# Performance work log

Measured on AMD Instinct MI355X. Metric: run time of the kernel, lower is better.

The kernel has to match this reference:

```python
import jax, jax.numpy as jnp
import numpy as np

PI = float(np.pi)
EPS = 1e-7


def conv2d(x, w, b, pad=0):
    y = jax.lax.conv_general_dilated(x, w, (1, 1), [(pad, pad), (pad, pad)],
                                     dimension_numbers=('NCHW', 'OIHW', 'NCHW'))
    return y + b[None, :, None, None]


def nearest_resize(x, oh, ow):
    # PyTorch F.interpolate(mode='nearest'): src_idx = floor(dst_idx * in/out)
    ih, iw = x.shape[-2], x.shape[-1]
    ri = (jnp.arange(oh) * ih) // oh
    ci = (jnp.arange(ow) * iw) // ow
    return x[:, :, ri, :][:, :, :, ci]


def maxpool_to(x, oh, ow):
    # adaptive_max_pool2d with divisible sizes == strided max pool
    b, c, h, w = x.shape
    return x.reshape(b, c, oh, h // oh, ow, w // ow).max(axis=(3, 5))


def minmax(t):
    # per-sample min-max normalization over (channel,h,w)
    mn = t.min(axis=(1, 2, 3), keepdims=True)
    mx = t.max(axis=(1, 2, 3), keepdims=True)
    return (t - mn) / (mx - mn + EPS)


def nonlocal2d(x, g_w, g_b, th_w, th_b, ph_w, ph_b, out_w, out_b):
    # embedded-Gaussian NonLocal2D, reduction=1, use_scale=False
    b, c, h, w = x.shape
    g_x = conv2d(x, g_w, g_b).reshape(b, c, h * w).transpose(0, 2, 1)    # (b, hw, c)
    th = conv2d(x, th_w, th_b).reshape(b, c, h * w).transpose(0, 2, 1)   # (b, hw, c)
    ph = conv2d(x, ph_w, ph_b).reshape(b, c, h * w)                      # (b, c, hw)
    pw = jax.nn.softmax(jnp.einsum('bic,bcj->bij', th, ph), axis=-1)     # (b, hw, hw)
    y = jnp.einsum('bij,bjc->bic', pw, g_x).transpose(0, 2, 1).reshape(b, c, h, w)
    return x + conv2d(y, out_w, out_b)


def reference(x0, x1, x2, x3, x4, rc_w, rc_b,
              nl_g_w, nl_g_b, nl_theta_w, nl_theta_b,
              nl_phi_w, nl_phi_b, nl_out_w, nl_out_b):
    inputs = [x0, x1, x2, x3, x4]
    refine_level = 2
    gh, gw = inputs[refine_level].shape[2:]
    feats = []
    for i, x in enumerate(inputs):
        if i < refine_level:
            feats.append(maxpool_to(x, gh, gw))
        else:
            feats.append(nearest_resize(x, gh, gw))
    ori_fe = sum(feats) / len(feats)
    bsf = nonlocal2d(ori_fe, nl_g_w, nl_g_b, nl_theta_w, nl_theta_b,
                     nl_phi_w, nl_phi_b, nl_out_w, nl_out_b)

    outs = []
    for i, x in enumerate(inputs):
        b, c, h, w = x.shape
        # ConvModule(C->1, 3x3, relu) then extra F.relu (idempotent)
        basic_map = jax.nn.relu(conv2d(x, rc_w[i], rc_b[i], pad=1))      # (b,1,h,w)
        row = x.mean(axis=3)[:, 0, :]                                     # (b,h)
        col = x.mean(axis=2)[:, 0, :]                                     # (b,w)
        avg_map = minmax((row[:, :, None] * col[:, None, :])[:, None])    # (b,1,h,w)
        basic_reg = minmax(basic_map)
        distance_map = jnp.cos((avg_map - basic_reg) * (PI / 2))
        attention = jax.nn.relu(nearest_resize(bsf, h, w) * distance_map)
        outs.append(x + attention)
    return tuple(outs)


def setup_inputs() -> dict:
    key = jax.random.key(0)
    ks = jax.random.split(key, 16)
    C = 256
    sizes = [200, 100, 50, 25, 13]
    inp = {}
    for i, s in enumerate(sizes):
        inp[f'x{i}'] = jax.random.normal(ks[i], (4, C, s, s), dtype=jnp.float32)
    inp['rc_w'] = jax.random.normal(ks[5], (5, 1, C, 3, 3), dtype=jnp.float32) * 0.02
    inp['rc_b'] = jnp.zeros((5, 1), dtype=jnp.float32)
    inp['nl_g_w'] = jax.random.normal(ks[6], (C, C, 1, 1), dtype=jnp.float32) * 0.02
    inp['nl_g_b'] = jnp.zeros((C,), dtype=jnp.float32)
    inp['nl_theta_w'] = jax.random.normal(ks[7], (C, C, 1, 1), dtype=jnp.float32) * 0.02
    inp['nl_theta_b'] = jnp.zeros((C,), dtype=jnp.float32)
    inp['nl_phi_w'] = jax.random.normal(ks[8], (C, C, 1, 1), dtype=jnp.float32) * 0.02
    inp['nl_phi_b'] = jnp.zeros((C,), dtype=jnp.float32)
    inp['nl_out_w'] = jax.random.normal(ks[9], (C, C, 1, 1), dtype=jnp.float32) * 0.02
    inp['nl_out_b'] = jnp.zeros((C,), dtype=jnp.float32)
    return inp
```

## Files before the change

kernel.cpp:

```cpp
#include <hip/hip_runtime.h>
#include <math.h>

typedef __attribute__((ext_vector_type(8))) short short8;
typedef __attribute__((ext_vector_type(4))) float f32x4;
typedef __attribute__((ext_vector_type(2))) float f32x2;
typedef __attribute__((ext_vector_type(4))) unsigned short u16x4;

#define EPSV 1e-7f
#define PI_2 1.57079632679489662f
#define NEG_BIG (-3.4e38f)

constexpr int B = 4, C = 256;
constexpr int GW = 50;
constexpr int PR = 2500, PP = 2560;
constexpr int CPP = C * PP;
constexpr long long SPB = (long long)PP * PP;
constexpr int PS = PP * C;
constexpr int ZT = 213176;

constexpr size_t OFF_ORI   = 0;
constexpr size_t OFF_BSF   = OFF_ORI + (size_t)B * CPP;
constexpr size_t OFF_Z     = OFF_BSF + (size_t)B * CPP;
constexpr size_t OFF_BASIC = OFF_Z + (size_t)9 * ZT;
constexpr size_t OFF_ROW   = OFF_BASIC + 213184;
constexpr size_t OFF_COL   = OFF_ROW + 1600;
constexpr size_t OFF_STATS = OFF_COL + 1600;
constexpr size_t OFF_RSUM  = OFF_STATS + 128;
constexpr size_t OFF_U16   = OFF_RSUM + 10240;
constexpr size_t U_ORIT = 0;
constexpr size_t U_THT  = U_ORIT + (size_t)B * CPP;
constexpr size_t U_PHT  = U_THT  + (size_t)B * CPP;
constexpr size_t U_G    = U_PHT  + (size_t)B * CPP;
constexpr size_t U_YTT  = U_G    + (size_t)B * CPP;
constexpr size_t U_WB   = U_YTT  + (size_t)B * CPP;

__device__ __forceinline__ unsigned short f2b(float x) {
    union { float f; unsigned u; } q{x};
    unsigned r = q.u + 0x7FFFu + ((q.u >> 16) & 1u);
    return (unsigned short)(r >> 16);
}
__device__ __forceinline__ float b2f(unsigned short u) {
    union { unsigned u; float f; } q{(unsigned)u << 16};
    return q.f;
}

__device__ __forceinline__ float orife_val(
    int idx, const float* __restrict__ x0, const float* __restrict__ x1,
    const float* __restrict__ x2, const float* __restrict__ x3,
    const float* __restrict__ x4)
{
    int p = idx % PP; int bc = idx / PP;
    if (p >= PR) return 0.0f;
    int y = p / GW, x = p % GW;
    const float* p0 = x0 + (size_t)bc * 40000;
    float m0 = NEG_BIG;
    #pragma unroll
    for (int dy = 0; dy < 4; dy++) {
        f32x4 r = *(const f32x4*)(p0 + (y * 4 + dy) * 200 + x * 4);
        m0 = fmaxf(m0, fmaxf(fmaxf(r[0], r[1]), fmaxf(r[2], r[3])));
    }
    const float* p1 = x1 + (size_t)bc * 10000;
    float m1 = fmaxf(fmaxf(p1[(y*2)*100 + x*2],   p1[(y*2)*100 + x*2+1]),
                     fmaxf(p1[(y*2+1)*100 + x*2], p1[(y*2+1)*100 + x*2+1]));
    float v2 = x2[(size_t)bc * 2500 + p];
    float v3 = x3[(size_t)bc * 625 + (y/2)*25 + (x/2)];
    int ry = (y * 13) / 50, rx = (x * 13) / 50;
    float v4 = x4[(size_t)bc * 169 + ry * 13 + rx];
    return (m0 + m1 + v2 + v3 + v4) * 0.2f;
}

constexpr int ORIFE_T = 2560 * 256;

__global__ __launch_bounds__(256) void k_pre(
    const float* __restrict__ x0, const float* __restrict__ x1,
    const float* __restrict__ x2, const float* __restrict__ x3,
    const float* __restrict__ x4, const float* __restrict__ rc_w,
    const float* __restrict__ wth, const float* __restrict__ wph,
    const float* __restrict__ wg,  const float* __restrict__ wout,
    unsigned short* __restrict__ wb, float* __restrict__ ori,
    float* __restrict__ z, float* __restrict__ row, float* __restrict__ col,
    float* __restrict__ rowsum)
{
    __shared__ float wsm[C * 12];
    const int bx = blockIdx.x;
    const int tid = threadIdx.x;

    if (bx < 388) {
        int rid = bx * 4 + (tid >> 6);
        int lane = tid & 63;
        int base, H; const float* x;
        if      (rid < 800)  { base = 0;    H = 200; x = x0; }
        else if (rid < 1200) { base = 800;  H = 100; x = x1; }
        else if (rid < 1400) { base = 1200; H = 50;  x = x2; }
        else if (rid < 1500) { base = 1400; H = 25;  x = x3; }
        else                 { base = 1500; H = 13;  x = x4; }
        int r = rid - base; int b = r / H, h = r - (r / H) * H;
        const float* xr = x + (size_t)b * C * H * H + (size_t)h * H;
        float s = 0.0f;
        for (int w = lane; w < H; w += 64) s += xr[w];
        #pragma unroll
        for (int off = 32; off > 0; off >>= 1) s += __shfl_down(s, off);
        if (lane == 0) row[rid] = s / (float)H;
    } else if (bx < 395) {
        int idx = (bx - 388) * 256 + tid;
        if (idx >= 1552) return;
        int base, H; const float* x;
        if      (idx < 800)  { base = 0;    H = 200; x = x0; }
        else if (idx < 1200) { base = 800;  H = 100; x = x1; }
        else if (idx < 1400) { base = 1200; H = 50;  x = x2; }
        else if (idx < 1500) { base = 1400; H = 25;  x = x3; }
        else                 { base = 1500; H = 13;  x = x4; }
        int r = idx - base; int b = r / H, w = r - (r / H) * H;
        const float* xc = x + (size_t)b * C * H * H + w;
        float s = 0.0f;
        int h = 0;
        for (; h + 3 < H; h += 4) {
            float a0 = xc[(size_t)h * H];
            float a1 = xc[(size_t)(h + 1) * H];
            float a2 = xc[(size_t)(h + 2) * H];
            float a3 = xc[(size_t)(h + 3) * H];
            s += (a0 + a1) + (a2 + a3);
        }
        for (; h < H; h++) s += xc[(size_t)h * H];
        col[idx] = s / (float)H;
    } else if (bx < 1419) {
        int idx = (bx - 395) * 256 + tid;
        int seg = idx >> 16, off = idx & 65535;
        const float* s = (seg == 0) ? wth : (seg == 1) ? wph : (seg == 2) ? wg : wout;
        wb[idx] = f2b(s[off]);
    } else if (bx < 1838) {
        int bxx = bx - 1419;
        int lvl, base, HW, PH, zb; const float* x;
        if      (bxx < 313) { lvl = 0; base = 0;   HW = 40000; PH = 20000; zb = 0;      x = x0; }
        else if (bxx < 392) { lvl = 1; base = 313; HW = 10000; PH = 5000;  zb = 160000; x = x1; }
        else if (bxx < 412) { lvl = 2; base = 392; HW = 2500;  PH = 1250;  zb = 200000; x = x2; }
        else if (bxx < 417) { lvl = 3; base = 412; HW = 625;   PH = 313;   zb = 210000; x = x3; }
        else                { lvl = 4; base = 417; HW = 169;   PH = 85;    zb = 212500; x = x4; }
        const bool alig = (HW & 1) == 0;

        const float* w9 = rc_w + (size_t)lvl * C * 9;
        for (int i = tid; i < C * 9; i += 256) wsm[(i / 9) * 12 + (i % 9)] = w9[i];
        __syncthreads();

        int idx = (bxx - base) * 256 + tid;
        if (idx >= B * PH) return;
        int b = idx / PH, pp = (idx - b * PH) * 2;
        bool has2 = (pp + 1 < HW);

        float acc0[9] = {}, acc1[9] = {};
        const float* xp = x + (size_t)b * C * HW + pp;
        for (int c0 = 0; c0 < C; c0 += 8) {
            float v0[8], v1[8];
            #pragma unroll
            for (int k = 0; k < 8; k++) {
                const float* a = xp + (size_t)(c0 + k) * HW;
                if (alig && has2) { f32x2 t = *(const f32x2*)a; v0[k] = t[0]; v1[k] = t[1]; }
                else { v0[k] = a[0]; v1[k] = has2 ? a[1] : 0.0f; }
            }
            #pragma unroll
            for (int k = 0; k < 8; k++) {
                const float* wc = &wsm[(c0 + k) * 12];
                f32x4 w0 = *(const f32x4*)wc;
                f32x4 w1 = *(const f32x4*)(wc + 4);
                float w8 = wc[8];
                acc0[0] += v0[k] * w0[0]; acc1[0] += v1[k] * w0[0];
                acc0[1] += v0[k] * w0[1]; acc1[1] += v1[k] * w0[1];
                acc0[2] += v0[k] * w0[2]; acc1[2] += v1[k] * w0[2];
                acc0[3] += v0[k] * w0[3]; acc1[3] += v1[k] * w0[3];
                acc0[4] += v0[k] * w1[0]; acc1[4] += v1[k] * w1[0];
                acc0[5] += v0[k] * w1[1]; acc1[5] += v1[k] * w1[1];
                acc0[6] += v0[k] * w1[2]; acc1[6] += v1[k] * w1[2];
                acc0[7] += v0[k] * w1[3]; acc1[7] += v1[k] * w1[3];
                acc0[8] += v0[k] * w8;    acc1[8] += v1[k] * w8;
            }
        }
        #pragma unroll
        for (int t = 0; t < 9; t++) {
            size_t o = (size_t)t * ZT + zb + (size_t)b * HW + pp;
            if (alig && has2) { f32x2 wv = {acc0[t], acc1[t]}; *(f32x2*)&z[o] = wv; }
            else { z[o] = acc0[t]; if (has2) z[o + 1] = acc1[t]; }
        }
    } else if (bx < 4398) {
        int t0 = (bx - 1838) * 256 + tid;
        #pragma unroll
        for (int k = 0; k < 4; k++) {
            int idx = t0 + k * ORIFE_T;
            ori[idx] = orife_val(idx, x0, x1, x2, x3, x4);
        }
    } else {
        int idx = (bx - 4398) * 1024 + tid * 4;
        f32x4 zv = {0.0f, 0.0f, 0.0f, 0.0f};
        *(f32x4*)(rowsum + idx) = zv;
    }
}

__global__ __launch_bounds__(256) void k_tcvt(const float* __restrict__ ori,
                                              unsigned short* __restrict__ ot)
{
    __shared__ unsigned short t[64][66];
    int p0 = blockIdx.x * 64, c0 = blockIdx.y * 64, b = blockIdx.z;
    int pp = threadIdx.x & 63, cb = threadIdx.x >> 6;
    #pragma unroll
    for (int i = 0; i < 16; i++) {
        int cc = cb * 16 + i;
        t[cc][pp] = f2b(ori[((size_t)b * C + c0 + cc) * PP + p0 + pp]);
    }
    __syncthreads();
    int cc2 = threadIdx.x & 63, pb = threadIdx.x >> 6;
    #pragma unroll
    for (int i = 0; i < 16; i++) {
        int pp2 = pb * 16 + i;
        ot[((size_t)b * PP + p0 + pp2) * C + c0 + cc2] = t[cc2][pp2];
    }
}

constexpr int LDT = 40;

__global__ __launch_bounds__(256) void k_proj(
    const unsigned short* __restrict__ wb, const unsigned short* __restrict__ orit,
    const float* __restrict__ th_b, const float* __restrict__ ph_b,
    const float* __restrict__ g_b,
    unsigned short* __restrict__ tht, unsigned short* __restrict__ pht,
    unsigned short* __restrict__ gb)
{
    __shared__ __align__(16) unsigned short As[128 * LDT];
    __shared__ __align__(16) unsigned short Bs[128 * LDT];

    const int z = blockIdx.z;
    const int b = z / 3, wsel = z - b * 3;
    const bool tp = (wsel < 2);
    const unsigned short* A = tp ? (orit + (size_t)b * CPP) : (wb + 131072);
    const unsigned short* Bm = tp ? (wb + wsel * 65536) : (orit + (size_t)b * CPP);
    const float* bias = (wsel == 0) ? th_b : (wsel == 1) ? ph_b : g_b;

    const int m0 = (tp ? blockIdx.x : blockIdx.y) * 128;
    const int n0 = (tp ? blockIdx.y : blockIdx.x) * 128;
    const int tid = threadIdx.x;
    const int lane = tid & 63, w = tid >> 6;
    const int wm = (w & 1) * 64, wn = (w >> 1) * 64;
    const int fr = lane & 15, fq = lane >> 4;

    f32x4 acc[4][4] = {};
    for (int k0 = 0; k0 < 256; k0 += 32) {
        #pragma unroll
        for (int l = 0; l < 2; l++) {
            int li = tid + l * 256;
            int rr = li >> 2, kc = li & 3;
            short8 va = *(const short8*)(A  + (size_t)(m0 + rr) * 256 + k0 + kc * 8);
            short8 vb = *(const short8*)(Bm + (size_t)(n0 + rr) * 256 + k0 + kc * 8);
            *(short8*)&As[rr * LDT + kc * 8] = va;
            *(short8*)&Bs[rr * LDT + kc * 8] = vb;
        }
        __syncthreads();
        short8 af[4], bf[4];
        #pragma unroll
        for (int i = 0; i < 4; i++)
            af[i] = *(const short8*)&As[(wm + i * 16 + fr) * LDT + fq * 8];
        #pragma unroll
        for (int j = 0; j < 4; j++)
            bf[j] = *(const short8*)&Bs[(wn + j * 16 + fr) * LDT + fq * 8];
        #pragma unroll
        for (int i = 0; i < 4; i++)
            #pragma unroll
            for (int j = 0; j < 4; j++)
                acc[i][j] = __builtin_amdgcn_mfma_f32_16x16x32_bf16(
                    af[i], bf[j], acc[i][j], 0, 0, 0);
        __syncthreads();
    }

    unsigned short* dst = (wsel == 0) ? tht : (wsel == 1) ? pht : gb;
    dst += (size_t)b * CPP;
    #pragma unroll
    for (int i = 0; i < 4; i++) {
        #pragma unroll
        for (int r = 0; r < 4; r++) {
            int gm = m0 + wm + i * 16 + fq * 4 + r;
            #pragma unroll
            for (int j = 0; j < 4; j++) {
                int gn = n0 + wn + j * 16 + fr;
                float v = acc[i][j][r] + (tp ? bias[gn] : bias[gm]);
                if (!tp && gn >= PR) v = 0.0f;
                size_t off = tp ? ((size_t)gm * 256 + gn) : ((size_t)gm * PP + gn);
                dst[off] = f2b(v);
            }
        }
    }
}

template<bool AddBias, bool AddRes, bool OutBf, bool OutExp, bool BParts>
__global__ __launch_bounds__(256) void k_bgemm(
    const unsigned short* __restrict__ A, const unsigned short* __restrict__ Bm,
    const float* __restrict__ bias, const float* __restrict__ res,
    void* __restrict__ Cout, int K, int lda, int ldb, int ldc,
    long long sA, long long sB, long long sC, long long sR,
    int nsplit, long long sK,
    float* __restrict__ rowsum, const float* __restrict__ parts)
{
    __shared__ __align__(16) unsigned short As[128 * LDT];
    __shared__ __align__(16) unsigned short Bs[128 * LDT];

    const int z = blockIdx.z;
    const int bz = z / nsplit, ks = z - bz * nsplit;
    A  += (size_t)sA * bz + (size_t)sK * ks;
    Bm += (size_t)sB * bz + (size_t)sK * ks;

    const int m0 = blockIdx.y * 128, n0 = blockIdx.x * 128;
    const int tid = threadIdx.x;
    const int lane = tid & 63, w = tid >> 6;
    const int wm = (w & 1) * 64, wn = (w >> 1) * 64;
    const int fr = lane & 15, fq = lane >> 4;

    float inv0 = 0.0f, inv1 = 0.0f;
    const float* pbase = nullptr;
    if constexpr (BParts) {
        pbase = parts + (size_t)(bz * 2) * PS;
        inv0 = 1.0f / rowsum[(size_t)bz * PP + n0 + (tid >> 2)];
        inv1 = 1.0f / rowsum[(size_t)bz * PP + n0 + ((tid + 256) >> 2)];
    }

    f32x4 acc[4][4] = {};
    for (int k0 = 0; k0 < K; k0 += 32) {
        #pragma unroll
        for (int l = 0; l < 2; l++) {
            int li = tid + l * 256;
            int rr = li >> 2, kc = li & 3;
            short8 va = *(const short8*)(A + (size_t)(m0 + rr) * lda + k0 + kc * 8);
            short8 vb;
            if constexpr (BParts) {
                const float* pb = pbase + (size_t)(n0 + rr) * 256 + k0 + kc * 8;
                f32x4 a0 = *(const f32x4*)pb;
                f32x4 a1 = *(const f32x4*)(pb + 4);
                f32x4 b0 = *(const f32x4*)(pb + PS);
                f32x4 b1 = *(const f32x4*)(pb + PS + 4);
                float inv = l ? inv1 : inv0;
                #pragma unroll
                for (int e = 0; e < 4; e++) {
                    vb[e]     = (short)f2b((a0[e] + b0[e]) * inv);
                    vb[e + 4] = (short)f2b((a1[e] + b1[e]) * inv);
                }
            } else {
                vb = *(const short8*)(Bm + (size_t)(n0 + rr) * ldb + k0 + kc * 8);
            }
            *(short8*)&As[rr * LDT + kc * 8] = va;
            *(short8*)&Bs[rr * LDT + kc * 8] = vb;
        }
        __syncthreads();
        short8 af[4], bf[4];
        #pragma unroll
        for (int i = 0; i < 4; i++)
            af[i] = *(const short8*)&As[(wm + i * 16 + fr) * LDT + fq * 8];
        #pragma unroll
        for (int j = 0; j < 4; j++)
            bf[j] = *(const short8*)&Bs[(wn + j * 16 + fr) * LDT + fq * 8];
        #pragma unroll
        for (int i = 0; i < 4; i++)
            #pragma unroll
            for (int j = 0; j < 4; j++)
                acc[i][j] = __builtin_amdgcn_mfma_f32_16x16x32_bf16(
                    af[i], bf[j], acc[i][j], 0, 0, 0);
        __syncthreads();
    }

    float* Cf = (float*)Cout;
    unsigned short* Cb = (unsigned short*)Cout;
    const size_t co = (size_t)sC * z;
    const size_t ro = (size_t)sR * bz;
    float rsacc[4][4] = {};
    #pragma unroll
    for (int i = 0; i < 4; i++) {
        #pragma unroll
        for (int r = 0; r < 4; r++) {
            int gm = m0 + wm + i * 16 + fq * 4 + r;
            #pragma unroll
            for (int j = 0; j < 4; j++) {
                int gn = n0 + wn + j * 16 + fr;
                float v = acc[i][j][r];
                if constexpr (AddBias) v += bias[gm];
                if constexpr (AddRes)  v += res[ro + (size_t)gm * ldc + gn];
                size_t off = co + (size_t)gm * ldc + gn;
                if constexpr (OutExp) {
                    float e = (gn < PR) ? __expf(v) : 0.0f;
                    Cb[off] = f2b(e);
                    rsacc[i][r] += e;
                } else if constexpr (OutBf) {
                    Cb[off] = f2b(v);
                } else {
                    Cf[off] = v;
                }
            }
        }
    }
    if constexpr (OutExp) {
        #pragma unroll
        for (int i = 0; i < 4; i++)
            #pragma unroll
            for (int r = 0; r < 4; r++) {
                float s = rsacc[i][r];
                s += __shfl_xor(s, 1);
                s += __shfl_xor(s, 2);
                s += __shfl_xor(s, 4);
                s += __shfl_xor(s, 8);
                if (fr == 0)
                    atomicAdd(&rowsum[(size_t)bz * PP + m0 + wm + i * 16 + fq * 4 + r], s);
            }
    }
}

template<int H, int ZB>
__device__ __forceinline__ void ccomb_impl(int idx, const float* __restrict__ z,
                                           float biasv, float* __restrict__ bas)
{
    constexpr int W = H, HW = H * W;
    int r = idx - ZB; int b = r / HW; int p = r - b * HW;
    int y = p / W, x = p - (p / W) * W;
    float acc = biasv;
    #pragma unroll
    for (int dy = 0; dy < 3; dy++) {
        int yy = y + dy - 1;
        if (yy < 0 || yy >= H) continue;
        #pragma unroll
        for (int dx = 0; dx < 3; dx++) {
            int xx = x + dx - 1;
            if (xx < 0 || xx >= W) continue;
            acc += z[(size_t)(dy * 3 + dx) * ZT + ZB + (size_t)b * HW + yy * W + xx];
        }
    }
    bas[idx] = fmaxf(acc, 0.0f);
}

__global__ __launch_bounds__(256) void k_ccomb_f(const float* __restrict__ z,
                                                 const float* __restrict__ rb,
                                                 float* __restrict__ bas)
{
    int idx = blockIdx.x * 256 + threadIdx.x;
    if (idx >= ZT) return;
    if      (idx < 160000) ccomb_impl<200, 0>     (idx, z, rb[0], bas);
    else if (idx < 200000) ccomb_impl<100, 160000>(idx, z, rb[1], bas);
    else if (idx < 210000) ccomb_impl<50,  200000>(idx, z, rb[2], bas);
    else if (idx < 212500) ccomb_impl<25,  210000>(idx, z, rb[3], bas);
    else                   ccomb_impl<13,  212500>(idx, z, rb[4], bas);
}

__global__ __launch_bounds__(256) void k_stats_f(
    const float* __restrict__ row, const float* __restrict__ col,
    const float* __restrict__ basic, float* __restrict__ stats)
{
    const int Ht[5]  = {200, 100, 50, 25, 13};
    const int ZBt[5] = {0, 160000, 200000, 210000, 212500};
    const int RBt[5] = {0, 800, 1200, 1400, 1500};
    int lvl = blockIdx.x >> 2, b = blockIdx.x & 3;
    int H = Ht[lvl], HW = H * H;
    const float* rw = row + RBt[lvl] + b * H;
    const float* cl = col + RBt[lvl] + b * H;
    const float* bb = basic + ZBt[lvl] + (size_t)b * HW;

    __shared__ float smn[256], smx[256];
    int t = threadIdx.x;
    float rmn, rmx, cmn, cmx, bmn, bmx;

    float mn = 3.4e38f, mx = NEG_BIG;
    for (int h = t; h < H; h += 256) { float v = rw[h]; mn = fminf(mn, v); mx = fmaxf(mx, v); }
    smn[t] = mn; smx[t] = mx; __syncthreads();
    for (int s = 128; s > 0; s >>= 1) { if (t < s) { smn[t] = fminf(smn[t], smn[t+s]); smx[t] = fmaxf(smx[t], smx[t+s]); } __syncthreads(); }
    rmn = smn[0]; rmx = smx[0]; __syncthreads();

    mn = 3.4e38f; mx = NEG_BIG;
    for (int w = t; w < H; w += 256) { float v = cl[w]; mn = fminf(mn, v); mx = fmaxf(mx, v); }
    smn[t] = mn; smx[t] = mx; __syncthreads();
    for (int s = 128; s > 0; s >>= 1) { if (t < s) { smn[t] = fminf(smn[t], smn[t+s]); smx[t] = fmaxf(smx[t], smx[t+s]); } __syncthreads(); }
    cmn = smn[0]; cmx = smx[0]; __syncthreads();

    mn = 3.4e38f; mx = NEG_BIG;
    for (int i = t; i < HW; i += 256) { float v = bb[i]; mn = fminf(mn, v); mx = fmaxf(mx, v); }
    smn[t] = mn; smx[t] = mx; __syncthreads();
    for (int s = 128; s > 0; s >>= 1) { if (t < s) { smn[t] = fminf(smn[t], smn[t+s]); smx[t] = fmaxf(smx[t], smx[t+s]); } __syncthreads(); }
    bmn = smn[0]; bmx = smx[0];

    if (t == 0) {
        float p1 = rmn * cmn, p2 = rmn * cmx, p3 = rmx * cmn, p4 = rmx * cmx;
        float amn = fminf(fminf(p1, p2), fminf(p3, p4));
        float amx = fmaxf(fmaxf(p1, p2), fmaxf(p3, p4));
        float* st = stats + lvl * 16 + b * 4;
        st[0] = amn; st[1] = amx; st[2] = bmn; st[3] = bmx;
    }
}

template<int H, int ZB, int RB, int LVL>
__device__ __forceinline__ void dist_impl(int idx, float* __restrict__ basic,
                                          const float* __restrict__ row,
                                          const float* __restrict__ col,
                                          const float* __restrict__ stats)
{
    constexpr int HW = H * H;
    int r = idx - ZB; int b = r / HW; int p = r - b * HW;
    int yh = p / H, xw = p - (p / H) * H;
    const float* st = stats + LVL * 16 + b * 4;
    float amn = st[0], amx = st[1], bmn = st[2], bmx = st[3];
    float an = (row[RB + b * H + yh] * col[RB + b * H + xw] - amn) / (amx - amn + EPSV);
    float bn = (basic[idx] - bmn) / (bmx - bmn + EPSV);
    basic[idx] = cosf((an - bn) * PI_2);
}

__global__ __launch_bounds__(256) void k_dist_f(float* __restrict__ basic,
                                                const float* __restrict__ row,
                                                const float* __restrict__ col,
                                                const float* __restrict__ stats)
{
    int idx = blockIdx.x * 256 + threadIdx.x;
    if (idx >= ZT) return;
    if      (idx < 160000) dist_impl<200, 0,      0,    0>(idx, basic, row, col, stats);
    else if (idx < 200000) dist_impl<100, 160000, 800,  1>(idx, basic, row, col, stats);
    else if (idx < 210000) dist_impl<50,  200000, 1200, 2>(idx, basic, row, col, stats);
    else if (idx < 212500) dist_impl<25,  210000, 1400, 3>(idx, basic, row, col, stats);
    else                   dist_impl<13,  212500, 1500, 4>(idx, basic, row, col, stats);
}

template<int LVL>
__device__ __forceinline__ void final_v4(int vid, const float* __restrict__ x,
                                         const unsigned short* __restrict__ bsf,
                                         const float* __restrict__ dist,
                                         float* __restrict__ out)
{
    constexpr int H = (LVL == 0) ? 200 : 100;
    constexpr int W = H, HW = H * W, Wv = W / 4;
    int xv = vid % Wv; int t = vid / Wv;
    int yh = t % H; t /= H; int c = t % C; int b = t / C;
    f32x4 xw4 = *(const f32x4*)(x + (size_t)vid * 4);
    f32x4 d4  = *(const f32x4*)(dist + (size_t)b * HW + yh * W + xv * 4);
    const unsigned short* bb = bsf + ((size_t)b * C + c) * PP;
    f32x4 o;
    if constexpr (LVL == 0) {
        float bv = b2f(bb[(yh >> 2) * GW + xv]);
        #pragma unroll
        for (int k = 0; k < 4; k++) o[k] = xw4[k] + fmaxf(bv * d4[k], 0.0f);
    } else {
        float bv0 = b2f(bb[(yh >> 1) * GW + 2 * xv]);
        float bv1 = b2f(bb[(yh >> 1) * GW + 2 * xv + 1]);
        o[0] = xw4[0] + fmaxf(bv0 * d4[0], 0.0f);
        o[1] = xw4[1] + fmaxf(bv0 * d4[1], 0.0f);
        o[2] = xw4[2] + fmaxf(bv1 * d4[2], 0.0f);
        o[3] = xw4[3] + fmaxf(bv1 * d4[3], 0.0f);
    }
    *(f32x4*)(out + (size_t)vid * 4) = o;
}

template<int LVL>
__device__ __forceinline__ void final_s(int idx, const float* __restrict__ x,
                                        const unsigned short* __restrict__ bsf,
                                        const float* __restrict__ dist,
                                        float* __restrict__ out)
{
    constexpr int H = (LVL == 2) ? 50 : (LVL == 3) ? 25 : 13;
    constexpr int W = H, HW = H * W;
    int xw = idx % W; int t = idx / W;
    int yh = t % H; t /= H; int c = t % C; int b = t / C;
    float d = dist[(size_t)b * HW + yh * W + xw];
    constexpr bool ident = (LVL == 2);
    int ry = ident ? yh : (yh * GW) / H;
    int rx = ident ? xw : (xw * GW) / W;
    float bv = b2f(bsf[((size_t)b * C + c) * PP + ry * GW + rx]);
    out[idx] = x[idx] + fmaxf(bv * d, 0.0f);
}

__global__ __launch_bounds__(256) void k_final_f(
    const float* __restrict__ x0, const float* __restrict__ x1,
    const float* __restrict__ x2, const float* __restrict__ x3,
    const float* __restrict__ x4, const unsigned short* __restrict__ bsf,
    const float* __restrict__ basic, float* __restrict__ out)
{
    int bx = blockIdx.x;
    int tid = threadIdx.x;
    if (bx < 8000) {
        int t0 = bx * 256 + tid;
        #pragma unroll
        for (int k = 0; k < 5; k++)
            final_v4<0>(t0 + k * 2048000, x0, bsf, basic, out);
    } else if (bx < 10000) {
        int t0 = (bx - 8000) * 256 + tid;
        #pragma unroll
        for (int k = 0; k < 5; k++)
            final_v4<1>(t0 + k * 512000, x1, bsf, basic + 160000, out + 40960000ull);
    } else if (bx < 12000) {
        int t0 = (bx - 10000) * 256 + tid;
        #pragma unroll
        for (int k = 0; k < 5; k++)
            final_s<2>(t0 + k * 512000, x2, bsf, basic + 200000, out + 51200000ull);
    } else if (bx < 12500) {
        int t0 = (bx - 12000) * 256 + tid;
        #pragma unroll
        for (int k = 0; k < 5; k++)
            final_s<3>(t0 + k * 128000, x3, bsf, basic + 210000, out + 53760000ull);
    } else {
        int t0 = (bx - 12500) * 256 + tid;
        #pragma unroll
        for (int k = 0; k < 4; k++)
            final_s<4>(t0 + k * 43264, x4, bsf, basic + 212500, out + 54400000ull);
    }
}

extern "C" void kernel_launch(void* const* d_in, const int* in_sizes, int n_in,
                              void* d_out, int out_size, void* d_ws, size_t ws_size,
                              hipStream_t stream)
{
    const float* x[5]; for (int i = 0; i < 5; i++) x[i] = (const float*)d_in[i];
    const float* rc_w  = (const float*)d_in[5];
    const float* rc_b  = (const float*)d_in[6];
    const float* g_b   = (const float*)d_in[8];
    const float* th_b  = (const float*)d_in[10];
    const float* ph_b  = (const float*)d_in[12];
    const float* out_b = (const float*)d_in[14];
    float* out = (float*)d_out;

    float* ws    = (float*)d_ws;
    float* ori   = ws + OFF_ORI;
    unsigned short* bsf = (unsigned short*)(ws + OFF_BSF);
    float* zbuf  = ws + OFF_Z;
    float* basic = ws + OFF_BASIC;
    float* rowb  = ws + OFF_ROW;
    float* colb  = ws + OFF_COL;
    float* stats = ws + OFF_STATS;
    float* rowsum = ws + OFF_RSUM;
    unsigned short* u16 = (unsigned short*)(ws + OFF_U16);
    unsigned short* orit = u16 + U_ORIT;
    unsigned short* tht  = u16 + U_THT;
    unsigned short* pht  = u16 + U_PHT;
    unsigned short* gb   = u16 + U_G;
    unsigned short* wb   = u16 + U_WB;
    unsigned short* wb_out = wb + 196608;

    unsigned short* P_all = (unsigned short*)out;
    float* part = out + 4 * SPB;

    k_pre<<<4408, 256, 0, stream>>>(
        x[0], x[1], x[2], x[3], x[4], rc_w,
        (const float*)d_in[9], (const float*)d_in[11],
        (const float*)d_in[7], (const float*)d_in[13],
        wb, ori, zbuf, rowb, colb, rowsum);

    k_tcvt<<<dim3(PP / 64, C / 64, B), 256, 0, stream>>>(ori, orit);

    k_proj<<<dim3(20, 2, 12), 256, 0, stream>>>(wb, orit, th_b, ph_b, g_b, tht, pht, gb);

    k_ccomb_f<<<(ZT + 255) / 256, 256, 0, stream>>>(zbuf, rc_b, basic);
    k_stats_f<<<20, 256, 0, stream>>>(rowb, colb, basic, stats);
    k_dist_f<<<(ZT + 255) / 256, 256, 0, stream>>>(basic, rowb, colb, stats);

    dim3 gsc(PP / 128, PP / 128, B);
    k_bgemm<false, false, false, true, false><<<gsc, 256, 0, stream>>>(
        tht, pht, nullptr, nullptr, P_all, C, C, C, PP, CPP, CPP, SPB, 0, 1, 0,
        rowsum, nullptr);

    dim3 gyt(C / 128, PP / 128, B * 2);
    k_bgemm<false, false, false, false, false><<<gyt, 256, 0, stream>>>(
        P_all, gb, nullptr, nullptr, part, PP / 2, PP, PP, C, SPB, CPP, PS, 0, 2, PP / 2,
        nullptr, nullptr);

    dim3 gbsf(PP / 128, C / 128, B);
    k_bgemm<true, true, true, false, true><<<gbsf, 256, 0, stream>>>(
        wb_out, (const unsigned short*)part, out_b, ori, bsf, C, C, 0, PP,
        0, 0, CPP, CPP, 1, 0, rowsum, part);

    k_final_f<<<12669, 256, 0, stream>>>(
        x[0], x[1], x[2], x[3], x[4], bsf, basic, out);
}
```

Baseline: 375.6 us.

## Use one pixel per thread in reduce-conv and fuse transpose with conv combine

The per-level 3x3 channel-reduction path in k_pre now gives each thread one pixel instead of two, which doubles its block count and drops the vector-load and alignment branches. The transpose/bf16-convert kernel and the 3x3 combine kernel are merged into a single k_mid launch that dispatches on block index. This removes one kernel launch and gives the conv more parallelism. In exchange each thread does less work and the input loads become scalar.

```diff
diff --git a/kernel.cpp b/kernel.cpp
--- a/kernel.cpp
+++ b/kernel.cpp
@@ -3,7 +3,6 @@
 
 typedef __attribute__((ext_vector_type(8))) short short8;
 typedef __attribute__((ext_vector_type(4))) float f32x4;
-typedef __attribute__((ext_vector_type(2))) float f32x2;
 typedef __attribute__((ext_vector_type(4))) unsigned short u16x4;
 
 #define EPSV 1e-7f
@@ -128,89 +127,115 @@
         int seg = idx >> 16, off = idx & 65535;
         const float* s = (seg == 0) ? wth : (seg == 1) ? wph : (seg == 2) ? wg : wout;
         wb[idx] = f2b(s[off]);
-    } else if (bx < 1838) {
+    } else if (bx < 2254) {
         int bxx = bx - 1419;
-        int lvl, base, HW, PH, zb; const float* x;
-        if      (bxx < 313) { lvl = 0; base = 0;   HW = 40000; PH = 20000; zb = 0;      x = x0; }
-        else if (bxx < 392) { lvl = 1; base = 313; HW = 10000; PH = 5000;  zb = 160000; x = x1; }
-        else if (bxx < 412) { lvl = 2; base = 392; HW = 2500;  PH = 1250;  zb = 200000; x = x2; }
-        else if (bxx < 417) { lvl = 3; base = 412; HW = 625;   PH = 313;   zb = 210000; x = x3; }
-        else                { lvl = 4; base = 417; HW = 169;   PH = 85;    zb = 212500; x = x4; }
-        const bool alig = (HW & 1) == 0;
+        int lvl, base, HW, zb; const float* x;
+        if      (bxx < 625) { lvl = 0; base = 0;   HW = 40000; zb = 0;      x = x0; }
+        else if (bxx < 782) { lvl = 1; base = 625; HW = 10000; zb = 160000; x = x1; }
+        else if (bxx < 822) { lvl = 2; base = 782; HW = 2500;  zb = 200000; x = x2; }
+        else if (bxx < 832) { lvl = 3; base = 822; HW = 625;   zb = 210000; x = x3; }
+        else                { lvl = 4; base = 832; HW = 169;   zb = 212500; x = x4; }
 
         const float* w9 = rc_w + (size_t)lvl * C * 9;
         for (int i = tid; i < C * 9; i += 256) wsm[(i / 9) * 12 + (i % 9)] = w9[i];
         __syncthreads();
 
         int idx = (bxx - base) * 256 + tid;
-        if (idx >= B * PH) return;
-        int b = idx / PH, pp = (idx - b * PH) * 2;
-        bool has2 = (pp + 1 < HW);
-
-        float acc0[9] = {}, acc1[9] = {};
-        const float* xp = x + (size_t)b * C * HW + pp;
+        if (idx >= B * HW) return;
+        int b = idx / HW, p = idx - b * HW;
+
+        float acc[9] = {};
+        const float* xp = x + (size_t)b * C * HW + p;
         for (int c0 = 0; c0 < C; c0 += 8) {
-            float v0[8], v1[8];
+            float v[8];
             #pragma unroll
-            for (int k = 0; k < 8; k++) {
-                const float* a = xp + (size_t)(c0 + k) * HW;
-                if (alig && has2) { f32x2 t = *(const f32x2*)a; v0[k] = t[0]; v1[k] = t[1]; }
-                else { v0[k] = a[0]; v1[k] = has2 ? a[1] : 0.0f; }
-            }
+            for (int k = 0; k < 8; k++) v[k] = xp[(size_t)(c0 + k) * HW];
             #pragma unroll
             for (int k = 0; k < 8; k++) {
                 const float* wc = &wsm[(c0 + k) * 12];
                 f32x4 w0 = *(const f32x4*)wc;
                 f32x4 w1 = *(const f32x4*)(wc + 4);
                 float w8 = wc[8];
-                acc0[0] += v0[k] * w0[0]; acc1[0] += v1[k] * w0[0];
-                acc0[1] += v0[k] * w0[1]; acc1[1] += v1[k] * w0[1];
-                acc0[2] += v0[k] * w0[2]; acc1[2] += v1[k] * w0[2];
-                acc0[3] += v0[k] * w0[3]; acc1[3] += v1[k] * w0[3];
-                acc0[4] += v0[k] * w1[0]; acc1[4] += v1[k] * w1[0];
-                acc0[5] += v0[k] * w1[1]; acc1[5] += v1[k] * w1[1];
-                acc0[6] += v0[k] * w1[2]; acc1[6] += v1[k] * w1[2];
-                acc0[7] += v0[k] * w1[3]; acc1[7] += v1[k] * w1[3];
-                acc0[8] += v0[k] * w8;    acc1[8] += v1[k] * w8;
+                acc[0] += v[k] * w0[0]; acc[1] += v[k] * w0[1];
+                acc[2] += v[k] * w0[2]; acc[3] += v[k] * w0[3];
+                acc[4] += v[k] * w1[0]; acc[5] += v[k] * w1[1];
+                acc[6] += v[k] * w1[2]; acc[7] += v[k] * w1[3];
+                acc[8] += v[k] * w8;
             }
         }
         #pragma unroll
-        for (int t = 0; t < 9; t++) {
-            size_t o = (size_t)t * ZT + zb + (size_t)b * HW + pp;
-            if (alig && has2) { f32x2 wv = {acc0[t], acc1[t]}; *(f32x2*)&z[o] = wv; }
-            else { z[o] = acc0[t]; if (has2) z[o + 1] = acc1[t]; }
-        }
-    } else if (bx < 4398) {
-        int t0 = (bx - 1838) * 256 + tid;
+        for (int t = 0; t < 9; t++)
+            z[(size_t)t * ZT + zb + idx] = acc[t];
+    } else if (bx < 4814) {
+        int t0 = (bx - 2254) * 256 + tid;
         #pragma unroll
         for (int k = 0; k < 4; k++) {
             int idx = t0 + k * ORIFE_T;
             ori[idx] = orife_val(idx, x0, x1, x2, x3, x4);
         }
     } else {
-        int idx = (bx - 4398) * 1024 + tid * 4;
+        int idx = (bx - 4814) * 1024 + tid * 4;
         f32x4 zv = {0.0f, 0.0f, 0.0f, 0.0f};
         *(f32x4*)(rowsum + idx) = zv;
     }
 }
 
-__global__ __launch_bounds__(256) void k_tcvt(const float* __restrict__ ori,
-                                              unsigned short* __restrict__ ot)
+template<int H, int ZB>
+__device__ __forceinline__ void ccomb_impl(int idx, const float* __restrict__ z,
+                                           float biasv, float* __restrict__ bas)
+{
+    constexpr int W = H, HW = H * W;
+    int r = idx - ZB; int b = r / HW; int p = r - b * HW;
+    int y = p / W, x = p - (p / W) * W;
+    float acc = biasv;
+    #pragma unroll
+    for (int dy = 0; dy < 3; dy++) {
+        int yy = y + dy - 1;
+        if (yy < 0 || yy >= H) continue;
+        #pragma unroll
+        for (int dx = 0; dx < 3; dx++) {
+            int xx = x + dx - 1;
+            if (xx < 0 || xx >= W) continue;
+            acc += z[(size_t)(dy * 3 + dx) * ZT + ZB + (size_t)b * HW + yy * W + xx];
+        }
+    }
+    bas[idx] = fmaxf(acc, 0.0f);
+}
+
+__global__ __launch_bounds__(256) void k_mid(
+    const float* __restrict__ ori, unsigned short* __restrict__ ot,
+    const float* __restrict__ z, const float* __restrict__ rb,
+    float* __restrict__ bas)
 {
     __shared__ unsigned short t[64][66];
-    int p0 = blockIdx.x * 64, c0 = blockIdx.y * 64, b = blockIdx.z;
-    int pp = threadIdx.x & 63, cb = threadIdx.x >> 6;
-    #pragma unroll
-    for (int i = 0; i < 16; i++) {
-        int cc = cb * 16 + i;
-        t[cc][pp] = f2b(ori[((size_t)b * C + c0 + cc) * PP + p0 + pp]);
-    }
-    __syncthreads();
-    int cc2 = threadIdx.x & 63, pb = threadIdx.x >> 6;
-    #pragma unroll
-    for (int i = 0; i < 16; i++) {
-        int pp2 = pb * 16 + i;
-        ot[((size_t)b * PP + p0 + pp2) * C + c0 + cc2] = t[cc2][pp2];
+    const int bx = blockIdx.x;
+    const int tid = threadIdx.x;
+
+    if (bx < 640) {
+        int p0 = (bx % 40) * 64;
+        int c0 = ((bx / 40) & 3) * 64;
+        int b  = bx / 160;
+        int pp = tid & 63, cb = tid >> 6;
+        #pragma unroll
+        for (int i = 0; i < 16; i++) {
+            int cc = cb * 16 + i;
+            t[cc][pp] = f2b(ori[((size_t)b * C + c0 + cc) * PP + p0 + pp]);
+        }
+        __syncthreads();
+        int cc2 = tid & 63, pb = tid >> 6;
+        #pragma unroll
+        for (int i = 0; i < 16; i++) {
+            int pp2 = pb * 16 + i;
+            ot[((size_t)b * PP + p0 + pp2) * C + c0 + cc2] = t[cc2][pp2];
+        }
+    } else {
+        int idx = (bx - 640) * 256 + tid;
+        if (idx >= ZT) return;
+        if      (idx < 160000) ccomb_impl<200, 0>     (idx, z, rb[0], bas);
+        else if (idx < 200000) ccomb_impl<100, 160000>(idx, z, rb[1], bas);
+        else if (idx < 210000) ccomb_impl<50,  200000>(idx, z, rb[2], bas);
+        else if (idx < 212500) ccomb_impl<25,  210000>(idx, z, rb[3], bas);
+        else                   ccomb_impl<13,  212500>(idx, z, rb[4], bas);
     }
 }
 
@@ -406,41 +431,6 @@
     }
 }
 
-template<int H, int ZB>
-__device__ __forceinline__ void ccomb_impl(int idx, const float* __restrict__ z,
-                                           float biasv, float* __restrict__ bas)
-{
-    constexpr int W = H, HW = H * W;
-    int r = idx - ZB; int b = r / HW; int p = r - b * HW;
-    int y = p / W, x = p - (p / W) * W;
-    float acc = biasv;
-    #pragma unroll
-    for (int dy = 0; dy < 3; dy++) {
-        int yy = y + dy - 1;
-        if (yy < 0 || yy >= H) continue;
-        #pragma unroll
-        for (int dx = 0; dx < 3; dx++) {
-            int xx = x + dx - 1;
-            if (xx < 0 || xx >= W) continue;
-            acc += z[(size_t)(dy * 3 + dx) * ZT + ZB + (size_t)b * HW + yy * W + xx];
-        }
-    }
-    bas[idx] = fmaxf(acc, 0.0f);
-}
-
-__global__ __launch_bounds__(256) void k_ccomb_f(const float* __restrict__ z,
-                                                 const float* __restrict__ rb,
-                                                 float* __restrict__ bas)
-{
-    int idx = blockIdx.x * 256 + threadIdx.x;
-    if (idx >= ZT) return;
-    if      (idx < 160000) ccomb_impl<200, 0>     (idx, z, rb[0], bas);
-    else if (idx < 200000) ccomb_impl<100, 160000>(idx, z, rb[1], bas);
-    else if (idx < 210000) ccomb_impl<50,  200000>(idx, z, rb[2], bas);
-    else if (idx < 212500) ccomb_impl<25,  210000>(idx, z, rb[3], bas);
-    else                   ccomb_impl<13,  212500>(idx, z, rb[4], bas);
-}
-
 __global__ __launch_bounds__(256) void k_stats_f(
     const float* __restrict__ row, const float* __restrict__ col,
     const float* __restrict__ basic, float* __restrict__ stats)
@@ -631,17 +621,16 @@
     unsigned short* P_all = (unsigned short*)out;
     float* part = out + 4 * SPB;
 
-    k_pre<<<4408, 256, 0, stream>>>(
+    k_pre<<<4824, 256, 0, stream>>>(
         x[0], x[1], x[2], x[3], x[4], rc_w,
         (const float*)d_in[9], (const float*)d_in[11],
         (const float*)d_in[7], (const float*)d_in[13],
         wb, ori, zbuf, rowb, colb, rowsum);
 
-    k_tcvt<<<dim3(PP / 64, C / 64, B), 256, 0, stream>>>(ori, orit);
+    k_mid<<<1473, 256, 0, stream>>>(ori, orit, zbuf, rc_b, basic);
 
     k_proj<<<dim3(20, 2, 12), 256, 0, stream>>>(wb, orit, th_b, ph_b, g_b, tht, pht, gb);
 
-    k_ccomb_f<<<(ZT + 255) / 256, 256, 0, stream>>>(zbuf, rc_b, basic);
     k_stats_f<<<20, 256, 0, stream>>>(rowb, colb, basic, stats);
     k_dist_f<<<(ZT + 255) / 256, 256, 0, stream>>>(basic, rowb, colb, stats);
 
```

Measured after the change: 335.0 us. 1.12x faster.
